# Optimization experiments

Hardware: AMD Instinct MI355X
Metric: run time of the kernel (lower is better)

The kernel has to match this reference:

```python
import jax, jax.numpy as jnp
import numpy as np

NUM_GROUPS = 32
EPS = 1e-6


def group_norm(x, w, b):
    # x: (B, C, L); normalize per group of C//32 channels over (channels-in-group, L)
    B, C, L = x.shape
    xg = x.reshape(B, NUM_GROUPS, C // NUM_GROUPS, L)
    mean = jnp.mean(xg, axis=(2, 3), keepdims=True)
    var = jnp.var(xg, axis=(2, 3), keepdims=True)
    xn = ((xg - mean) * jax.lax.rsqrt(var + EPS)).reshape(B, C, L)
    return xn * w[None, :, None] + b[None, :, None]


def conv1x1(x, w, b):
    # 1x1 Conv1d == channel-mixing linear. x: (B,C,L), w: (O,C), b: (O,)
    return jnp.einsum('oc,bcl->bol', w, x) + b[None, :, None]


def setup_inputs() -> dict:
    key = jax.random.key(0)
    ks = jax.random.split(key, 6)
    B, C, L = 8, 512, 2048
    s = 1.0 / np.sqrt(C)
    return {
        'x': jax.random.normal(ks[0], (B, C, L), dtype=jnp.float32),
        'gn_w': jnp.ones((C,), jnp.float32),
        'gn_b': jnp.zeros((C,), jnp.float32),
        'wq': jax.random.normal(ks[1], (C, C), dtype=jnp.float32) * s,
        'bq': jnp.zeros((C,), jnp.float32),
        'wk': jax.random.normal(ks[2], (C, C), dtype=jnp.float32) * s,
        'bk': jnp.zeros((C,), jnp.float32),
        'wv': jax.random.normal(ks[3], (C, C), dtype=jnp.float32) * s,
        'bv': jnp.zeros((C,), jnp.float32),
        'wo': jax.random.normal(ks[4], (C, C), dtype=jnp.float32) * s,
        'bo': jnp.zeros((C,), jnp.float32),
    }


def reference(x, gn_w, gn_b, wq, bq, wk, bk, wv, bv, wo, bo):
    B, C, L = x.shape
    h = group_norm(x, gn_w, gn_b)
    q = conv1x1(h, wq, bq)  # (B,C,L)
    k = conv1x1(h, wk, bk)
    v = conv1x1(h, wv, bv)
    scale = jnp.asarray(C, x.dtype) ** -0.5
    # scores over length: w[b,i,j] = sum_c q[b,c,i] k[b,c,j]
    w_ = jnp.einsum('bci,bcj->bij', q, k) * scale
    w_ = jax.nn.softmax(w_, axis=-1)
    # h[b,c,i] = sum_j w[b,i,j] v[b,c,j]
    h = jnp.einsum('bij,bcj->bci', w_, v)
    h = conv1x1(h, wo, bo)
    return x + h
```

## Files before the change

### kernel.cpp

```cpp
#include <hip/hip_runtime.h>
#include <math.h>

#define BATCH 8
#define CH 512
#define LEN 2048
#define NG 32
#define CPG 16

typedef unsigned short u16;
typedef __bf16 bf16x8 __attribute__((ext_vector_type(8)));
typedef float f32x16 __attribute__((ext_vector_type(16)));

__device__ __forceinline__ u16 f2bf(float f) {
    union { float f; unsigned u; } c; c.f = f;
    unsigned r = c.u + 0x7fffu + ((c.u >> 16) & 1u);
    return (u16)(r >> 16);
}
__device__ __forceinline__ float bf2f(u16 h) {
    union { unsigned u; float f; } c; c.u = ((unsigned)h) << 16;
    return c.f;
}
__device__ __forceinline__ void gload16(const u16* g, u16* l) {
    __builtin_amdgcn_global_load_lds(
        (const __attribute__((address_space(1))) unsigned int*)g,
        (__attribute__((address_space(3))) unsigned int*)l, 16, 0, 0);
}

__global__ __launch_bounds__(256) void zerof4(float4* __restrict__ p) {
    p[blockIdx.x * 256 + threadIdx.x] = make_float4(0.f, 0.f, 0.f, 0.f);
}

__global__ __launch_bounds__(256) void wconv4(const float* __restrict__ w0, const float* __restrict__ w1,
                                              const float* __restrict__ w2, const float* __restrict__ w3,
                                              u16* __restrict__ o0, u16* __restrict__ o1,
                                              u16* __restrict__ o2, u16* __restrict__ o3) {
    const float* s; u16* d;
    switch (blockIdx.y) {
        case 0: s = w0; d = o0; break;
        case 1: s = w1; d = o1; break;
        case 2: s = w2; d = o2; break;
        default: s = w3; d = o3; break;
    }
    const int i = blockIdx.x * 256 + threadIdx.x;
    float4 f = ((const float4*)s)[i];
    ushort4 o = make_ushort4(f2bf(f.x), f2bf(f.y), f2bf(f.z), f2bf(f.w));
    ((ushort4*)d)[i] = o;
}

__global__ __launch_bounds__(256) void gn_stats(const float* __restrict__ x,
                                                const float* __restrict__ gw,
                                                const float* __restrict__ gb,
                                                float* __restrict__ gnA,
                                                float* __restrict__ gnB) {
    const int b = blockIdx.x >> 5, g = blockIdx.x & 31;
    const float4* xp = (const float4*)(x + ((size_t)b * CH + (size_t)g * CPG) * LEN);
    float s = 0.f, s2 = 0.f;
    for (int i = threadIdx.x; i < (CPG * LEN) / 4; i += 256) {
        float4 v = xp[i];
        s += v.x + v.y + v.z + v.w;
        s2 = fmaf(v.x, v.x, fmaf(v.y, v.y, fmaf(v.z, v.z, fmaf(v.w, v.w, s2))));
    }
    #pragma unroll
    for (int off = 32; off > 0; off >>= 1) {
        s  += __shfl_down(s, off, 64);
        s2 += __shfl_down(s2, off, 64);
    }
    __shared__ float sm[2][4];
    const int lane = threadIdx.x & 63, wv = threadIdx.x >> 6;
    if (lane == 0) { sm[0][wv] = s; sm[1][wv] = s2; }
    __syncthreads();
    if (threadIdx.x < CPG) {
        const float S  = sm[0][0] + sm[0][1] + sm[0][2] + sm[0][3];
        const float S2 = sm[1][0] + sm[1][1] + sm[1][2] + sm[1][3];
        const float mean = S * (1.f / (CPG * LEN));
        const float var  = S2 * (1.f / (CPG * LEN)) - mean * mean;
        const float rstd = rsqrtf(var + 1e-6f);
        const int c = g * CPG + threadIdx.x;
        const float sc = rstd * gw[c];
        gnA[b * CH + c] = sc;
        gnB[b * CH + c] = gb[c] - mean * sc;
    }
}

__global__ __launch_bounds__(256) void gn_apply_t(const float* __restrict__ x,
                                                  const float* __restrict__ gnA,
                                                  const float* __restrict__ gnB,
                                                  u16* __restrict__ Ht) {
    __shared__ float tile[64][65];
    const int b = blockIdx.z, c0 = blockIdx.y * 64, l0 = blockIdx.x * 64;
    const int t = threadIdx.x, tl = t & 63, tr = t >> 6;
    #pragma unroll 4
    for (int i = 0; i < 16; ++i) {
        const int c = tr + i * 4;
        const float a = gnA[b * CH + c0 + c];
        const float sh = gnB[b * CH + c0 + c];
        tile[c][tl] = x[((size_t)b * CH + c0 + c) * LEN + l0 + tl] * a + sh;
    }
    __syncthreads();
    #pragma unroll 4
    for (int i = 0; i < 16; ++i) {
        const int l = tr + i * 4;
        Ht[((size_t)b * LEN + l0 + l) * CH + c0 + tl] = f2bf(tile[tl][l]);
    }
}

#define EPI_QK   0
#define EPI_TBN  1
#define EPI_EXP  2
#define EPI_TNRM 3
#define EPI_FIN  4

template <int MODE>
__global__ __launch_bounds__(256, 4) void gemm_bt(
    const u16* __restrict__ A, int lda, long long sA,
    const u16* __restrict__ B, int ldb, long long sB,
    void* __restrict__ Out, void* __restrict__ Out2,
    int ldo, long long sO,
    const float* __restrict__ bias, const float* __restrict__ bias2,
    const float* __restrict__ res, long long sR,
    float* __restrict__ rsum, long long sRS,
    int K, float alpha) {
    __shared__ u16 As[128 * 64];
    __shared__ u16 Bs[128 * 64];
    const int b = blockIdx.z;
    const int n0 = blockIdx.x * 128, m0 = blockIdx.y * 128;
    A += (size_t)b * sA;
    B += (size_t)b * sB;
    const int t = threadIdx.x;
    const int lane = t & 63, wid = t >> 6;

    const int rowL = t >> 3, kq = (t & 7) ^ (rowL & 7);
    unsigned aoff = (unsigned)((m0 + rowL) * lda + kq * 8);
    unsigned boff = (unsigned)((n0 + rowL) * ldb + kq * 8);
    u16* const lds_dst_a = As + t * 8;
    u16* const lds_dst_b = Bs + t * 8;

    f32x16 acc[2][2];
    #pragma unroll
    for (int i = 0; i < 2; ++i)
        #pragma unroll
        for (int j = 0; j < 2; ++j)
            acc[i][j] = (f32x16)(0.f);

    const int col = lane & 31, half = lane >> 5;
    const int wm = (wid & 1) * 64, wn = (wid >> 1) * 64;
    const int mf = wm + col, nf = wn + col;
    const int mswz = mf & 7, nswz = nf & 7;

    for (int k0 = 0; k0 < K; k0 += 64) {
        #pragma unroll
        for (int g = 0; g < 4; ++g) {
            gload16(A + aoff + g * (32 * lda), lds_dst_a + g * 2048);
            gload16(B + boff + g * (32 * ldb), lds_dst_b + g * 2048);
        }
        aoff += 64; boff += 64;
        __syncthreads();
        #pragma unroll
        for (int ks = 0; ks < 4; ++ks) {
            const int kcA = ((ks * 2 + half) ^ mswz) * 8;
            const int kcB = ((ks * 2 + half) ^ nswz) * 8;
            bf16x8 a0 = *(const bf16x8*)(As + (mf)      * 64 + kcA);
            bf16x8 a1 = *(const bf16x8*)(As + (mf + 32) * 64 + kcA);
            bf16x8 b0 = *(const bf16x8*)(Bs + (nf)      * 64 + kcB);
            bf16x8 b1 = *(const bf16x8*)(Bs + (nf + 32) * 64 + kcB);
            acc[0][0] = __builtin_amdgcn_mfma_f32_32x32x16_bf16(a0, b0, acc[0][0], 0, 0, 0);
            acc[0][1] = __builtin_amdgcn_mfma_f32_32x32x16_bf16(a0, b1, acc[0][1], 0, 0, 0);
            acc[1][0] = __builtin_amdgcn_mfma_f32_32x32x16_bf16(a1, b0, acc[1][0], 0, 0, 0);
            acc[1][1] = __builtin_amdgcn_mfma_f32_32x32x16_bf16(a1, b1, acc[1][1], 0, 0, 0);
        }
        __syncthreads();
    }

    if (MODE == EPI_FIN) {
        float* O = (float*)Out + (size_t)b * sO;
        const float* R = res + (size_t)b * sR;
        #pragma unroll
        for (int im = 0; im < 2; ++im)
            #pragma unroll
            for (int g4 = 0; g4 < 4; ++g4) {
                const int mb = m0 + wm + im * 32 + g4 * 8 + half * 4;
                #pragma unroll
                for (int jn = 0; jn < 2; ++jn) {
                    const int n = n0 + wn + jn * 32 + col;
                    const float bb = bias[n];
                    const size_t base = (size_t)n * ldo + mb;
                    const float4 r4 = *(const float4*)&R[base];
                    float4 o4;
                    o4.x = acc[im][jn][g4 * 4 + 0] + bb + r4.x;
                    o4.y = acc[im][jn][g4 * 4 + 1] + bb + r4.y;
                    o4.z = acc[im][jn][g4 * 4 + 2] + bb + r4.z;
                    o4.w = acc[im][jn][g4 * 4 + 3] + bb + r4.w;
                    *(float4*)&O[base] = o4;
                }
            }
    } else if (MODE == EPI_EXP) {
        u16* O = (u16*)Out + (size_t)b * sO;
        float* RS = rsum + (size_t)b * sRS;
        float psum[2] = {0.f, 0.f};
        #pragma unroll
        for (int im = 0; im < 2; ++im)
            #pragma unroll
            for (int g4 = 0; g4 < 4; ++g4) {
                const int mb = m0 + wm + im * 32 + g4 * 8 + half * 4;
                #pragma unroll
                for (int jn = 0; jn < 2; ++jn) {
                    const int n = n0 + wn + jn * 32 + col;
                    u16 h0 = f2bf(__expf(acc[im][jn][g4 * 4 + 0] * alpha));
                    u16 h1 = f2bf(__expf(acc[im][jn][g4 * 4 + 1] * alpha));
                    u16 h2 = f2bf(__expf(acc[im][jn][g4 * 4 + 2] * alpha));
                    u16 h3 = f2bf(__expf(acc[im][jn][g4 * 4 + 3] * alpha));
                    psum[jn] += bf2f(h0) + bf2f(h1) + bf2f(h2) + bf2f(h3);
                    *(ushort4*)&O[(size_t)n * ldo + mb] = make_ushort4(h0, h1, h2, h3);
                }
            }
        #pragma unroll
        for (int jn = 0; jn < 2; ++jn) psum[jn] += __shfl_xor(psum[jn], 32, 64);
        if (half == 0) {
            #pragma unroll
            for (int jn = 0; jn < 2; ++jn)
                atomicAdd(&RS[n0 + wn + jn * 32 + col], psum[jn]);
        }
    } else {
        u16* O;
        const float* bi = bias;
        const float* RS = (MODE == EPI_TNRM) ? rsum + (size_t)b * sRS : nullptr;
        int mbase = m0 + wm;
        if (MODE == EPI_QK) {
            const bool hi = (m0 & 512) != 0;
            O  = (u16*)(hi ? Out2 : Out) + (size_t)b * sO;
            bi = hi ? bias2 : bias;
            mbase = (m0 & 511) + wm;
        } else {
            O = (u16*)Out + (size_t)b * sO;
        }
        float inv[2];
        if (MODE == EPI_TNRM) {
            inv[0] = 1.f / RS[n0 + wn + col];
            inv[1] = 1.f / RS[n0 + wn + 32 + col];
        }
        #pragma unroll
        for (int im = 0; im < 2; ++im)
            #pragma unroll
            for (int g4 = 0; g4 < 4; ++g4) {
                const int mb = mbase + im * 32 + g4 * 8 + half * 4;
                float4 bm = make_float4(0.f, 0.f, 0.f, 0.f);
                if (MODE == EPI_QK) bm = *(const float4*)&bi[mb];
                #pragma unroll
                for (int jn = 0; jn < 2; ++jn) {
                    const int n = n0 + wn + jn * 32 + col;
                    float v0 = acc[im][jn][g4 * 4 + 0];
                    float v1 = acc[im][jn][g4 * 4 + 1];
                    float v2 = acc[im][jn][g4 * 4 + 2];
                    float v3 = acc[im][jn][g4 * 4 + 3];
                    if (MODE == EPI_QK)  { v0 += bm.x; v1 += bm.y; v2 += bm.z; v3 += bm.w; }
                    if (MODE == EPI_TBN) { const float bb = bi[n]; v0 += bb; v1 += bb; v2 += bb; v3 += bb; }
                    if (MODE == EPI_TNRM) { v0 *= inv[jn]; v1 *= inv[jn]; v2 *= inv[jn]; v3 *= inv[jn]; }
                    ushort4 pk = make_ushort4(f2bf(v0), f2bf(v1), f2bf(v2), f2bf(v3));
                    *(ushort4*)&O[(size_t)n * ldo + mb] = pk;
                }
            }
    }
}

extern "C" void kernel_launch(void* const* d_in, const int* in_sizes, int n_in,
                              void* d_out, int out_size, void* d_ws, size_t ws_size,
                              hipStream_t stream) {
    const float* x    = (const float*)d_in[0];
    const float* gn_w = (const float*)d_in[1];
    const float* gn_b = (const float*)d_in[2];
    const float* wq   = (const float*)d_in[3];
    const float* bq   = (const float*)d_in[4];
    const float* wk   = (const float*)d_in[5];
    const float* bk   = (const float*)d_in[6];
    const float* wv   = (const float*)d_in[7];
    const float* bv   = (const float*)d_in[8];
    const float* wo   = (const float*)d_in[9];
    const float* bo   = (const float*)d_in[10];
    float* out = (float*)d_out;

    char* p = (char*)d_ws;
    const size_t WSZ = (size_t)CH * CH * 2;
    const size_t HSZ = (size_t)BATCH * CH * LEN * 2;
    u16* Wqk = (u16*)p; p += 2 * WSZ;
    u16* Wvb = (u16*)p; p += WSZ;
    u16* Wob = (u16*)p; p += WSZ;
    u16* Ht  = (u16*)p; p += HSZ;
    u16* Qt  = (u16*)p; p += HSZ;
    u16* Kt  = (u16*)p; p += HSZ;
    u16* Vb  = (u16*)p; p += HSZ;
    u16* Sb  = (u16*)p; p += (size_t)BATCH * LEN * LEN * 2;
    float* gnA = (float*)p; p += (size_t)BATCH * CH * 4;
    float* gnB = (float*)p; p += (size_t)BATCH * CH * 4;
    float* rowsum = (float*)p;

    const long long sH = (long long)LEN * CH;
    const long long sV = (long long)CH * LEN;
    const long long sS = (long long)LEN * LEN;
    const float scale = 0.04419417382415922f;

    wconv4<<<dim3(256, 4), 256, 0, stream>>>(wq, wk, wv, wo,
                                             Wqk, Wqk + (size_t)CH * CH, Wvb, Wob);
    gn_stats<<<BATCH * NG, 256, 0, stream>>>(x, gn_w, gn_b, gnA, gnB);
    gn_apply_t<<<dim3(LEN / 64, CH / 64, BATCH), 256, 0, stream>>>(x, gnA, gnB, Ht);
    zerof4<<<BATCH * LEN / 1024, 256, 0, stream>>>((float4*)rowsum);

    gemm_bt<EPI_QK><<<dim3(16, 8, 8), 256, 0, stream>>>(
        Wqk, CH, 0, Ht, CH, sH, Qt, Kt, CH, sH, bq, bk, nullptr, 0, nullptr, 0, CH, 0.f);
    gemm_bt<EPI_TBN><<<dim3(4, 16, 8), 256, 0, stream>>>(
        Ht, CH, sH, Wvb, CH, 0, Vb, nullptr, LEN, sV, bv, nullptr, nullptr, 0, nullptr, 0, CH, 0.f);
    gemm_bt<EPI_EXP><<<dim3(16, 16, 8), 256, 0, stream>>>(
        Kt, CH, sH, Qt, CH, sH, Sb, nullptr, LEN, sS, nullptr, nullptr, nullptr, 0, rowsum, LEN, CH, scale);
    gemm_bt<EPI_TNRM><<<dim3(16, 4, 8), 256, 0, stream>>>(
        Vb, LEN, sV, Sb, LEN, sS, Ht, nullptr, CH, sH, nullptr, nullptr, nullptr, 0, rowsum, LEN, LEN, 0.f);
    gemm_bt<EPI_FIN><<<dim3(4, 16, 8), 256, 0, stream>>>(
        Ht, CH, sH, Wob, CH, 0, out, nullptr, LEN, sV, bo, nullptr, x, sV, nullptr, 0, CH, 0.f);
}
```

Baseline: 287.4 us.

## Add 256x256 eight-wave double-buffered GEMM for QK projection and score kernels

Introduces a new gemm8p kernel with 512 threads, 256x256 output tiles, double-buffered LDS staging via global_load_lds, and a four-phase schedule that interleaves prefetch with MFMA under s_setprio. It also remaps block indices across XCD-style groups of eight. The QK projection and the exp(scores) GEMM now use it, while the old kernel keeps only the other modes. The larger tiles are meant to raise data reuse and overlap loads with compute, at the cost of more LDS and registers per block and fewer blocks in flight.

```diff
diff --git a/kernel.cpp b/kernel.cpp
--- a/kernel.cpp
+++ b/kernel.cpp
@@ -25,6 +25,12 @@
         (const __attribute__((address_space(1))) unsigned int*)g,
         (__attribute__((address_space(3))) unsigned int*)l, 16, 0, 0);
 }
+
+#define BARRIER() do {                                   \
+    asm volatile("" ::: "memory");                       \
+    __builtin_amdgcn_s_barrier();                        \
+    asm volatile("" ::: "memory");                       \
+} while (0)
 
 __global__ __launch_bounds__(256) void zerof4(float4* __restrict__ p) {
     p[blockIdx.x * 256 + threadIdx.x] = make_float4(0.f, 0.f, 0.f, 0.f);
@@ -109,6 +115,158 @@
 #define EPI_EXP  2
 #define EPI_TNRM 3
 #define EPI_FIN  4
+
+template <int MODE>
+__global__ __launch_bounds__(512, 2) void gemm8p(
+    const u16* __restrict__ A, int lda, long long sA,
+    const u16* __restrict__ B, int ldb, long long sB,
+    void* __restrict__ Out, void* __restrict__ Out2,
+    int ldo, long long sO,
+    const float* __restrict__ bias, const float* __restrict__ bias2,
+    float* __restrict__ rsum, long long sRS,
+    int K, float alpha) {
+    __shared__ u16 As[2][256 * 64];
+    __shared__ u16 Bs[2][256 * 64];
+
+    const int gx = gridDim.x, gy = gridDim.y;
+    int flat = (blockIdx.z * gy + blockIdx.y) * gx + blockIdx.x;
+    const int nbk = gx * gy * (int)gridDim.z;
+    flat = (flat & 7) * (nbk >> 3) + (flat >> 3);
+    const int bz = flat / (gx * gy);
+    const int rr = flat - bz * gx * gy;
+    const int by = rr / gx;
+    const int bx = rr - by * gx;
+
+    const int n0 = bx * 256, m0 = by * 256;
+    A += (size_t)bz * sA;
+    B += (size_t)bz * sB;
+
+    const int t = threadIdx.x;
+    const int lane = t & 63, wid = t >> 6;
+    const int col = lane & 31, half = lane >> 5;
+    const int wm = (wid >> 2) * 128, wn = (wid & 3) * 64;
+    const int cswz = col & 7;
+
+    const int rowL = t >> 3;
+    const int kq8 = ((t & 7) ^ (rowL & 7)) * 8;
+    unsigned aoff[4], boff[4];
+    #pragma unroll
+    for (int u = 0; u < 4; ++u) {
+        aoff[u] = (unsigned)((m0 + u * 64 + rowL) * lda + kq8);
+        boff[u] = (unsigned)((n0 + u * 64 + rowL) * ldb + kq8);
+    }
+    const int dst = t * 8;
+
+    f32x16 acc[4][2];
+    #pragma unroll
+    for (int mi = 0; mi < 4; ++mi)
+        #pragma unroll
+        for (int nj = 0; nj < 2; ++nj)
+            acc[mi][nj] = (f32x16)(0.f);
+
+    auto stA = [&](int u, unsigned ko, u16* buf) { gload16(A + aoff[u] + ko, buf + u * 4096 + dst); };
+    auto stB = [&](int u, unsigned ko, u16* buf) { gload16(B + boff[u] + ko, buf + u * 4096 + dst); };
+
+#define PHASE(QM, QN, STG, W1, W2) do {                                             \
+    bf16x8 av0[4], av1[4], bv[4];                                                   \
+    _Pragma("unroll")                                                               \
+    for (int ks = 0; ks < 4; ++ks) {                                                \
+        const int sl = ((ks * 2 + half) ^ cswz) * 8;                                \
+        av0[ks] = *(const bf16x8*)(Ac + (wm + (QM) * 64      + col) * 64 + sl);     \
+        av1[ks] = *(const bf16x8*)(Ac + (wm + (QM) * 64 + 32 + col) * 64 + sl);     \
+        bv[ks]  = *(const bf16x8*)(Bc + (wn + (QN) * 32 + col) * 64 + sl);          \
+    }                                                                               \
+    STG; W1;                                                                        \
+    BARRIER();                                                                      \
+    __builtin_amdgcn_s_setprio(1);                                                  \
+    _Pragma("unroll")                                                               \
+    for (int ks = 0; ks < 4; ++ks) {                                                \
+        acc[(QM)*2+0][QN] = __builtin_amdgcn_mfma_f32_32x32x16_bf16(av0[ks], bv[ks], acc[(QM)*2+0][QN], 0, 0, 0); \
+        acc[(QM)*2+1][QN] = __builtin_amdgcn_mfma_f32_32x32x16_bf16(av1[ks], bv[ks], acc[(QM)*2+1][QN], 0, 0, 0); \
+    }                                                                               \
+    __builtin_amdgcn_s_setprio(0);                                                  \
+    W2;                                                                             \
+    BARRIER();                                                                      \
+} while (0)
+
+    stB(0, 0, Bs[0]); stB(1, 0, Bs[0]); stB(2, 0, Bs[0]); stB(3, 0, Bs[0]);
+    stA(0, 0, As[0]); stA(2, 0, As[0]); stA(1, 0, As[0]); stA(3, 0, As[0]);
+    asm volatile("s_waitcnt vmcnt(2)" ::: "memory");
+    BARRIER();
+
+    const int NT = K >> 6;
+    for (int kt = 0; kt < NT; ++kt) {
+        const u16* Ac = As[kt & 1];
+        const u16* Bc = Bs[kt & 1];
+        u16* An = As[(kt + 1) & 1];
+        u16* Bn = Bs[(kt + 1) & 1];
+        const bool pf = (kt + 1 < NT);
+        const unsigned ko = (unsigned)((kt + 1) << 6);
+
+        PHASE(0, 0,
+              if (pf) { stB(0, ko, Bn); stB(1, ko, Bn); },
+              if (pf) { asm volatile("s_waitcnt vmcnt(2)" ::: "memory"); }
+              else    { asm volatile("s_waitcnt vmcnt(0)" ::: "memory"); }, );
+        PHASE(1, 0,
+              if (pf) { stB(2, ko, Bn); stB(3, ko, Bn); }, , );
+        PHASE(0, 1,
+              if (pf) { stA(0, ko, An); stA(2, ko, An); }, , );
+        PHASE(1, 1,
+              if (pf) { stA(1, ko, An); stA(3, ko, An); }, ,
+              if (pf) { asm volatile("s_waitcnt vmcnt(2)" ::: "memory"); });
+    }
+#undef PHASE
+
+    if (MODE == EPI_EXP) {
+        u16* O = (u16*)Out + (size_t)bz * sO;
+        float* RS = rsum + (size_t)bz * sRS;
+        float psum[2] = {0.f, 0.f};
+        #pragma unroll
+        for (int im = 0; im < 4; ++im)
+            #pragma unroll
+            for (int g4 = 0; g4 < 4; ++g4) {
+                const int mb = m0 + wm + im * 32 + g4 * 8 + half * 4;
+                #pragma unroll
+                for (int jn = 0; jn < 2; ++jn) {
+                    const int n = n0 + wn + jn * 32 + col;
+                    u16 h0 = f2bf(__expf(acc[im][jn][g4 * 4 + 0] * alpha));
+                    u16 h1 = f2bf(__expf(acc[im][jn][g4 * 4 + 1] * alpha));
+                    u16 h2 = f2bf(__expf(acc[im][jn][g4 * 4 + 2] * alpha));
+                    u16 h3 = f2bf(__expf(acc[im][jn][g4 * 4 + 3] * alpha));
+                    psum[jn] += bf2f(h0) + bf2f(h1) + bf2f(h2) + bf2f(h3);
+                    *(ushort4*)&O[(size_t)n * ldo + mb] = make_ushort4(h0, h1, h2, h3);
+                }
+            }
+        #pragma unroll
+        for (int jn = 0; jn < 2; ++jn) psum[jn] += __shfl_xor(psum[jn], 32, 64);
+        if (half == 0) {
+            #pragma unroll
+            for (int jn = 0; jn < 2; ++jn)
+                atomicAdd(&RS[n0 + wn + jn * 32 + col], psum[jn]);
+        }
+    } else {
+        const bool hi = (m0 & 512) != 0;
+        u16* O = (u16*)(hi ? Out2 : Out) + (size_t)bz * sO;
+        const float* bi = hi ? bias2 : bias;
+        const int mbase = (m0 & 511) + wm;
+        #pragma unroll
+        for (int im = 0; im < 4; ++im)
+            #pragma unroll
+            for (int g4 = 0; g4 < 4; ++g4) {
+                const int mb = mbase + im * 32 + g4 * 8 + half * 4;
+                const float4 bm = *(const float4*)&bi[mb];
+                #pragma unroll
+                for (int jn = 0; jn < 2; ++jn) {
+                    const int n = n0 + wn + jn * 32 + col;
+                    ushort4 pk = make_ushort4(f2bf(acc[im][jn][g4 * 4 + 0] + bm.x),
+                                              f2bf(acc[im][jn][g4 * 4 + 1] + bm.y),
+                                              f2bf(acc[im][jn][g4 * 4 + 2] + bm.z),
+                                              f2bf(acc[im][jn][g4 * 4 + 3] + bm.w));
+                    *(ushort4*)&O[(size_t)n * ldo + mb] = pk;
+                }
+            }
+    }
+}
 
 template <int MODE>
 __global__ __launch_bounds__(256, 4) void gemm_bt(
@@ -193,46 +351,11 @@
                     *(float4*)&O[base] = o4;
                 }
             }
-    } else if (MODE == EPI_EXP) {
+    } else {
         u16* O = (u16*)Out + (size_t)b * sO;
-        float* RS = rsum + (size_t)b * sRS;
-        float psum[2] = {0.f, 0.f};
-        #pragma unroll
-        for (int im = 0; im < 2; ++im)
-            #pragma unroll
-            for (int g4 = 0; g4 < 4; ++g4) {
-                const int mb = m0 + wm + im * 32 + g4 * 8 + half * 4;
-                #pragma unroll
-                for (int jn = 0; jn < 2; ++jn) {
-                    const int n = n0 + wn + jn * 32 + col;
-                    u16 h0 = f2bf(__expf(acc[im][jn][g4 * 4 + 0] * alpha));
-                    u16 h1 = f2bf(__expf(acc[im][jn][g4 * 4 + 1] * alpha));
-                    u16 h2 = f2bf(__expf(acc[im][jn][g4 * 4 + 2] * alpha));
-                    u16 h3 = f2bf(__expf(acc[im][jn][g4 * 4 + 3] * alpha));
-                    psum[jn] += bf2f(h0) + bf2f(h1) + bf2f(h2) + bf2f(h3);
-                    *(ushort4*)&O[(size_t)n * ldo + mb] = make_ushort4(h0, h1, h2, h3);
-                }
-            }
-        #pragma unroll
-        for (int jn = 0; jn < 2; ++jn) psum[jn] += __shfl_xor(psum[jn], 32, 64);
-        if (half == 0) {
-            #pragma unroll
-            for (int jn = 0; jn < 2; ++jn)
-                atomicAdd(&RS[n0 + wn + jn * 32 + col], psum[jn]);
-        }
-    } else {
-        u16* O;
         const float* bi = bias;
         const float* RS = (MODE == EPI_TNRM) ? rsum + (size_t)b * sRS : nullptr;
-        int mbase = m0 + wm;
-        if (MODE == EPI_QK) {
-            const bool hi = (m0 & 512) != 0;
-            O  = (u16*)(hi ? Out2 : Out) + (size_t)b * sO;
-            bi = hi ? bias2 : bias;
-            mbase = (m0 & 511) + wm;
-        } else {
-            O = (u16*)Out + (size_t)b * sO;
-        }
+        const int mbase = m0 + wm;
         float inv[2];
         if (MODE == EPI_TNRM) {
             inv[0] = 1.f / RS[n0 + wn + col];
@@ -243,8 +366,6 @@
             #pragma unroll
             for (int g4 = 0; g4 < 4; ++g4) {
                 const int mb = mbase + im * 32 + g4 * 8 + half * 4;
-                float4 bm = make_float4(0.f, 0.f, 0.f, 0.f);
-                if (MODE == EPI_QK) bm = *(const float4*)&bi[mb];
                 #pragma unroll
                 for (int jn = 0; jn < 2; ++jn) {
                     const int n = n0 + wn + jn * 32 + col;
@@ -252,7 +373,6 @@
                     float v1 = acc[im][jn][g4 * 4 + 1];
                     float v2 = acc[im][jn][g4 * 4 + 2];
                     float v3 = acc[im][jn][g4 * 4 + 3];
-                    if (MODE == EPI_QK)  { v0 += bm.x; v1 += bm.y; v2 += bm.z; v3 += bm.w; }
                     if (MODE == EPI_TBN) { const float bb = bi[n]; v0 += bb; v1 += bb; v2 += bb; v3 += bb; }
                     if (MODE == EPI_TNRM) { v0 *= inv[jn]; v1 *= inv[jn]; v2 *= inv[jn]; v3 *= inv[jn]; }
                     ushort4 pk = make_ushort4(f2bf(v0), f2bf(v1), f2bf(v2), f2bf(v3));
@@ -304,12 +424,12 @@
     gn_apply_t<<<dim3(LEN / 64, CH / 64, BATCH), 256, 0, stream>>>(x, gnA, gnB, Ht);
     zerof4<<<BATCH * LEN / 1024, 256, 0, stream>>>((float4*)rowsum);
 
-    gemm_bt<EPI_QK><<<dim3(16, 8, 8), 256, 0, stream>>>(
-        Wqk, CH, 0, Ht, CH, sH, Qt, Kt, CH, sH, bq, bk, nullptr, 0, nullptr, 0, CH, 0.f);
+    gemm8p<EPI_QK><<<dim3(8, 4, 8), 512, 0, stream>>>(
+        Wqk, CH, 0, Ht, CH, sH, Qt, Kt, CH, sH, bq, bk, nullptr, 0, CH, 0.f);
     gemm_bt<EPI_TBN><<<dim3(4, 16, 8), 256, 0, stream>>>(
         Ht, CH, sH, Wvb, CH, 0, Vb, nullptr, LEN, sV, bv, nullptr, nullptr, 0, nullptr, 0, CH, 0.f);
-    gemm_bt<EPI_EXP><<<dim3(16, 16, 8), 256, 0, stream>>>(
-        Kt, CH, sH, Qt, CH, sH, Sb, nullptr, LEN, sS, nullptr, nullptr, nullptr, 0, rowsum, LEN, CH, scale);
+    gemm8p<EPI_EXP><<<dim3(8, 8, 8), 512, 0, stream>>>(
+        Kt, CH, sH, Qt, CH, sH, Sb, nullptr, LEN, sS, nullptr, nullptr, rowsum, LEN, CH, scale);
     gemm_bt<EPI_TNRM><<<dim3(16, 4, 8), 256, 0, stream>>>(
         Vb, LEN, sV, Sb, LEN, sS, Ht, nullptr, CH, sH, nullptr, nullptr, nullptr, 0, rowsum, LEN, LEN, 0.f);
     gemm_bt<EPI_FIN><<<dim3(4, 16, 8), 256, 0, stream>>>(
```

After: 312.3 us. 1.09x slower.

## Remap GEMM block order across XCDs and use nontemporal epilogue stores

Applied to the files above, without the earlier changes.

Blocks of the batched GEMM are renumbered so that consecutive hardware block IDs, which are dealt round-robin across the 8 XCDs, map to contiguous tiles within one batch. Each XCD's L2 then shares A/B panels. For the TNRM mode the traversal goes column-major over M tiles. Epilogue output and residual accesses switch to nontemporal loads and stores to avoid polluting the cache. The remap assumes the total block count is divisible by 8, and nontemporal stores of the exp matrix could hurt if a later kernel reads it from L2.

```diff
diff --git a/kernel.cpp b/kernel.cpp
--- a/kernel.cpp
+++ b/kernel.cpp
@@ -1,5 +1,6 @@
 #include <hip/hip_runtime.h>
 #include <math.h>
+#include <string.h>
 
 #define BATCH 8
 #define CH 512
@@ -10,6 +11,7 @@
 typedef unsigned short u16;
 typedef __bf16 bf16x8 __attribute__((ext_vector_type(8)));
 typedef float f32x16 __attribute__((ext_vector_type(16)));
+typedef float f32x4v __attribute__((ext_vector_type(4)));
 
 __device__ __forceinline__ u16 f2bf(float f) {
     union { float f; unsigned u; } c; c.f = f;
@@ -24,6 +26,10 @@
     __builtin_amdgcn_global_load_lds(
         (const __attribute__((address_space(1))) unsigned int*)g,
         (__attribute__((address_space(3))) unsigned int*)l, 16, 0, 0);
+}
+__device__ __forceinline__ void nt_store_u4(ushort4 v, u16* p) {
+    union { ushort4 s; unsigned long long u; } cv; cv.s = v;
+    __builtin_nontemporal_store(cv.u, (unsigned long long*)p);
 }
 
 __global__ __launch_bounds__(256) void zerof4(float4* __restrict__ p) {
@@ -122,10 +128,23 @@
     int K, float alpha) {
     __shared__ u16 As[128 * 64];
     __shared__ u16 Bs[128 * 64];
-    const int b = blockIdx.z;
-    const int n0 = blockIdx.x * 128, m0 = blockIdx.y * 128;
-    A += (size_t)b * sA;
-    B += (size_t)b * sB;
+
+    const int gx = gridDim.x, gy = gridDim.y;
+    int flat = (blockIdx.z * gy + blockIdx.y) * gx + blockIdx.x;
+    const int nbk = gx * gy * (int)gridDim.z;
+    flat = (flat & 7) * (nbk >> 3) + (flat >> 3);
+    const int bz = flat / (gx * gy);
+    const int rr = flat - bz * gx * gy;
+    int by, bx;
+    if (MODE == EPI_TNRM) {
+        by = rr % gy; bx = rr / gy;
+    } else {
+        by = rr / gx; bx = rr % gx;
+    }
+
+    const int n0 = bx * 128, m0 = by * 128;
+    A += (size_t)bz * sA;
+    B += (size_t)bz * sB;
     const int t = threadIdx.x;
     const int lane = t & 63, wid = t >> 6;
 
@@ -172,8 +191,8 @@
     }
 
     if (MODE == EPI_FIN) {
-        float* O = (float*)Out + (size_t)b * sO;
-        const float* R = res + (size_t)b * sR;
+        float* O = (float*)Out + (size_t)bz * sO;
+        const float* R = res + (size_t)bz * sR;
         #pragma unroll
         for (int im = 0; im < 2; ++im)
             #pragma unroll
@@ -184,18 +203,18 @@
                     const int n = n0 + wn + jn * 32 + col;
                     const float bb = bias[n];
                     const size_t base = (size_t)n * ldo + mb;
-                    const float4 r4 = *(const float4*)&R[base];
-                    float4 o4;
+                    const f32x4v r4 = __builtin_nontemporal_load((const f32x4v*)&R[base]);
+                    f32x4v o4;
                     o4.x = acc[im][jn][g4 * 4 + 0] + bb + r4.x;
                     o4.y = acc[im][jn][g4 * 4 + 1] + bb + r4.y;
                     o4.z = acc[im][jn][g4 * 4 + 2] + bb + r4.z;
                     o4.w = acc[im][jn][g4 * 4 + 3] + bb + r4.w;
-                    *(float4*)&O[base] = o4;
+                    __builtin_nontemporal_store(o4, (f32x4v*)&O[base]);
                 }
             }
     } else if (MODE == EPI_EXP) {
-        u16* O = (u16*)Out + (size_t)b * sO;
-        float* RS = rsum + (size_t)b * sRS;
+        u16* O = (u16*)Out + (size_t)bz * sO;
+        float* RS = rsum + (size_t)bz * sRS;
         float psum[2] = {0.f, 0.f};
         #pragma unroll
         for (int im = 0; im < 2; ++im)
@@ -210,7 +229,7 @@
                     u16 h2 = f2bf(__expf(acc[im][jn][g4 * 4 + 2] * alpha));
                     u16 h3 = f2bf(__expf(acc[im][jn][g4 * 4 + 3] * alpha));
                     psum[jn] += bf2f(h0) + bf2f(h1) + bf2f(h2) + bf2f(h3);
-                    *(ushort4*)&O[(size_t)n * ldo + mb] = make_ushort4(h0, h1, h2, h3);
+                    nt_store_u4(make_ushort4(h0, h1, h2, h3), &O[(size_t)n * ldo + mb]);
                 }
             }
         #pragma unroll
@@ -223,15 +242,15 @@
     } else {
         u16* O;
         const float* bi = bias;
-        const float* RS = (MODE == EPI_TNRM) ? rsum + (size_t)b * sRS : nullptr;
+        const float* RS = (MODE == EPI_TNRM) ? rsum + (size_t)bz * sRS : nullptr;
         int mbase = m0 + wm;
         if (MODE == EPI_QK) {
             const bool hi = (m0 & 512) != 0;
-            O  = (u16*)(hi ? Out2 : Out) + (size_t)b * sO;
+            O  = (u16*)(hi ? Out2 : Out) + (size_t)bz * sO;
             bi = hi ? bias2 : bias;
             mbase = (m0 & 511) + wm;
         } else {
-            O = (u16*)Out + (size_t)b * sO;
+            O = (u16*)Out + (size_t)bz * sO;
         }
         float inv[2];
         if (MODE == EPI_TNRM) {
```

Result: slower. 471.1 us (+63.9%).
